# Kernel tuning notes

Measured on AMD Instinct MI355X. Metric: run time of the kernel, lower is better.

Reference implementation:

```python
import jax, jax.numpy as jnp
import numpy as np

B, C, N = 32, 128, 64
HID = 2 * C
STEEPNESS = 50.0


def _bitonic_layers(n):
    """Index pairs (a, b) for each compare-exchange layer of a bitonic sorting
    network, matching diffsort's bitonic_network construction."""
    num_blocks = int(np.log2(n))
    assert n == 2 ** num_blocks
    layers = []
    for block in range(num_blocks):
        for layer in range(block + 1):
            m = 2 ** (block - layer)
            a_idx, b_idx = [], []
            for i in range(0, n, 2 * m):
                for j in range(m):
                    ix = i + j
                    a, b = ix, ix + m
                    # alternate direction within bitonic blocks
                    if (ix // 2 ** (block + 1)) % 2 == 1:
                        a, b = b, a
                    a_idx.append(a)
                    b_idx.append(b)
            layers.append((np.asarray(a_idx), np.asarray(b_idx)))
    return layers

_LAYERS = _bitonic_layers(N)  # 21 layers for N=64


def _diff_sort(scores):
    """Differentiable bitonic sort (diffsort, distribution='cauchy').
    Returns (soft-sorted scores, soft permutation matrix P) with
    sorted = scores @ P; the module applies P via bmm(P, rows)."""
    b, n = scores.shape
    x = scores
    P = jnp.broadcast_to(jnp.eye(n, dtype=scores.dtype), (b, n, n))
    inv_pi = 1.0 / np.pi
    for a_idx, b_idx in _LAYERS:
        xa, xb = x[:, a_idx], x[:, b_idx]
        alpha = jnp.arctan((xb - xa) * STEEPNESS) * inv_pi + 0.5  # Cauchy CDF
        x = x.at[:, a_idx].set(alpha * xa + (1.0 - alpha) * xb)
        x = x.at[:, b_idx].set((1.0 - alpha) * xa + alpha * xb)
        Pa, Pb = P[:, :, a_idx], P[:, :, b_idx]
        al = alpha[:, None, :]
        P = P.at[:, :, a_idx].set(al * Pa + (1.0 - al) * Pb)
        P = P.at[:, :, b_idx].set((1.0 - al) * Pa + al * Pb)
    return x, P


def setup_inputs() -> dict:
    key = jax.random.key(0)
    ks = jax.random.split(key, 9)
    s = 0.05  # keep score magnitudes reasonable under steepness=50
    return {
        "x": jax.random.normal(ks[0], (B, C, N, N), jnp.float32),
        "w1": jax.random.normal(ks[1], (HID, C), jnp.float32) * s,
        "b1": jax.random.normal(ks[2], (HID,), jnp.float32) * s,
        "w2": jax.random.normal(ks[3], (HID, HID), jnp.float32) * s,
        "b2": jax.random.normal(ks[4], (HID,), jnp.float32) * s,
        "w_row": jax.random.normal(ks[5], (HID, N), jnp.float32) * s,
        "b_row": jax.random.normal(ks[6], (1,), jnp.float32) * s,
        "w_col": jax.random.normal(ks[7], (HID, N), jnp.float32) * s,
        "b_col": jax.random.normal(ks[8], (1,), jnp.float32) * s,
    }


def reference(x, w1, b1, w2, b2, w_row, b_row, w_col, b_col):
    # feat_extractor: two 1x1 convs (pointwise channel GEMMs) + ReLU
    h = jax.nn.relu(jnp.einsum('bchw,oc->bohw', x, w1) + b1[None, :, None, None])
    h = jax.nn.relu(jnp.einsum('bchw,oc->bohw', h, w2) + b2[None, :, None, None])

    # row branch: Conv1d(HID*N,1,1) over flattened (channel, width) per row
    row_scores = jnp.einsum('bchw,cw->bh', h, w_row) + b_row  # (B, N)
    _, p_row = _diff_sort(row_scores)
    x = jnp.einsum('bij,bcjk->bcik', p_row, x)  # bmm(P_row, x) per channel

    # col branch: Conv1d(HID*N,1,1) over flattened (channel, height) per column
    col_scores = jnp.einsum('bchw,ch->bw', h, w_col) + b_col  # (B, N)
    _, p_col = _diff_sort(col_scores)
    # original: bmm(P_col, x^T) then view as (B,C,N,N) with NO transpose back
    x = jnp.einsum('bij,bckj->bcik', p_col, x)
    return x
```

## Files before the change

### kernel.cpp

```cpp
#include <hip/hip_runtime.h>
#include <math.h>

#define B_    32
#define C_    128
#define N_    64
#define HID_  256
#define PIX_  4096
#define STEEP 50.0f
#define INV_PI 0.318309886183790671f
#define LDH   272
#define LDX   72

typedef unsigned short u16;
typedef __attribute__((ext_vector_type(8))) short bf16x8;
typedef __attribute__((ext_vector_type(4))) float f32x4;

__device__ __forceinline__ u16 f2bf(float f) {
    unsigned int u = __builtin_bit_cast(unsigned int, f);
    unsigned int r = (u + 0x7FFFu + ((u >> 16) & 1u)) >> 16;
    return (u16)r;
}
__device__ __forceinline__ float bf2f(u16 h) {
    unsigned int u = ((unsigned int)h) << 16;
    return __builtin_bit_cast(float, u);
}
__device__ __forceinline__ int h1_idx(int p, int k) {
    return p * LDH + (((k >> 3) + (p & 7)) & 31) * 8 + (k & 7);
}
__device__ __forceinline__ int x_idx(int p, int k) {
    return p * LDH + 128 + (((k >> 3) + (p & 7)) & 15) * 8 + (k & 7);
}

__global__ void k_prep(const float* __restrict__ w1, const float* __restrict__ w2,
                       u16* __restrict__ w1h, u16* __restrict__ w1l,
                       u16* __restrict__ w2h, u16* __restrict__ w2l,
                       float* __restrict__ col_s, const float* __restrict__ b_col) {
    int i = blockIdx.x * 256 + threadIdx.x;
    if (i < B_ * N_) col_s[i] = b_col[0];
    if (i < HID_ * C_) {
        float v = w1[i];
        u16 h = f2bf(v);
        w1h[i] = h;
        w1l[i] = f2bf(v - bf2f(h));
    } else {
        int j = i - HID_ * C_;
        if (j < HID_ * HID_) {
            float v = w2[j];
            u16 h = f2bf(v);
            w2h[j] = h;
            w2l[j] = f2bf(v - bf2f(h));
        }
    }
}

__global__ __launch_bounds__(256) void k12_fused(
    const float* __restrict__ x,
    const u16* __restrict__ w1h, const u16* __restrict__ w1l,
    const float* __restrict__ b1,
    const u16* __restrict__ w2h, const u16* __restrict__ w2l,
    const float* __restrict__ b2, const float* __restrict__ w_row,
    const float* __restrict__ b_row, const float* __restrict__ w_col,
    float* __restrict__ row_s, float* __restrict__ col_s) {
    __shared__ __align__(16) u16 Lh[64 * LDH];
    __shared__ __align__(16) u16 Ll[64 * LDH];
    __shared__ float col_red[64];
    __shared__ float row_red;

    const int t = threadIdx.x;
    const int l = t & 63, w = t >> 6;
    const int col = l & 15, q = l >> 4;
    const int hrow = blockIdx.x;
    const int b = blockIdx.y;
    const float* xb = x + (size_t)b * C_ * PIX_ + hrow * 64;

    if (t < 64) col_red[t] = 0.f;
    if (t == 0) row_red = 0.f;

    {
        const int pt = t & 15, ct = t >> 4;
#pragma unroll
        for (int cc = 0; cc < 4; cc++) {
            const int c = cc * 32 + 2 * ct;
            float4 v0 = *(const float4*)&xb[(size_t)c * PIX_ + pt * 4];
            float4 v1 = *(const float4*)&xb[(size_t)(c + 1) * PIX_ + pt * 4];
            float a0[4] = {v0.x, v0.y, v0.z, v0.w};
            float a1[4] = {v1.x, v1.y, v1.z, v1.w};
#pragma unroll
            for (int j = 0; j < 4; j++) {
                int p = pt * 4 + j;
                u16 h0 = f2bf(a0[j]), h1v = f2bf(a1[j]);
                u16 l0 = f2bf(a0[j] - bf2f(h0)), l1 = f2bf(a1[j] - bf2f(h1v));
                int idx = x_idx(p, c);
                *(unsigned int*)&Lh[idx] = (unsigned int)h0 | ((unsigned int)h1v << 16);
                *(unsigned int*)&Ll[idx] = (unsigned int)l0 | ((unsigned int)l1 << 16);
            }
        }
    }
    __syncthreads();

    f32x4 acc[4][4];
#pragma unroll
    for (int i = 0; i < 4; i++)
#pragma unroll
        for (int j = 0; j < 4; j++) acc[i][j] = (f32x4){0.f, 0.f, 0.f, 0.f};

    bf16x8 ah[4], al_[4];
#pragma unroll
    for (int mf = 0; mf < 4; mf++) {
        size_t ro = (size_t)(64 * w + 16 * mf + col) * C_ + q * 8;
        ah[mf] = *(const bf16x8*)&w1h[ro];
        al_[mf] = *(const bf16x8*)&w1l[ro];
    }
#pragma unroll
    for (int kc = 0; kc < 4; kc++) {
        bf16x8 bh[4], bl[4];
#pragma unroll
        for (int nt = 0; nt < 4; nt++) {
            int idx = x_idx(nt * 16 + col, kc * 32 + q * 8);
            bh[nt] = *(const bf16x8*)&Lh[idx];
            bl[nt] = *(const bf16x8*)&Ll[idx];
        }
        bf16x8 ahn[4], aln[4];
        const int kn = (kc + 1) & 3;
#pragma unroll
        for (int mf = 0; mf < 4; mf++) {
            size_t ro = (size_t)(64 * w + 16 * mf + col) * C_ + kn * 32 + q * 8;
            ahn[mf] = *(const bf16x8*)&w1h[ro];
            aln[mf] = *(const bf16x8*)&w1l[ro];
        }
#pragma unroll
        for (int mf = 0; mf < 4; mf++)
#pragma unroll
            for (int nt = 0; nt < 4; nt++) {
                acc[mf][nt] = __builtin_amdgcn_mfma_f32_16x16x32_bf16(ah[mf], bh[nt], acc[mf][nt], 0, 0, 0);
                acc[mf][nt] = __builtin_amdgcn_mfma_f32_16x16x32_bf16(ah[mf], bl[nt], acc[mf][nt], 0, 0, 0);
                acc[mf][nt] = __builtin_amdgcn_mfma_f32_16x16x32_bf16(al_[mf], bh[nt], acc[mf][nt], 0, 0, 0);
            }
#pragma unroll
        for (int mf = 0; mf < 4; mf++) { ah[mf] = ahn[mf]; al_[mf] = aln[mf]; }
    }

    bf16x8 ah2[4], al2[4];
#pragma unroll
    for (int mf = 0; mf < 4; mf++) {
        size_t ro = (size_t)(64 * w + 16 * mf + col) * HID_ + q * 8;
        ah2[mf] = *(const bf16x8*)&w2h[ro];
        al2[mf] = *(const bf16x8*)&w2l[ro];
    }
    __syncthreads();

#pragma unroll
    for (int mf = 0; mf < 4; mf++) {
        int o = 64 * w + 16 * mf + q * 4;
        float bias[4];
#pragma unroll
        for (int r = 0; r < 4; r++) bias[r] = b1[o + r];
#pragma unroll
        for (int nt = 0; nt < 4; nt++) {
            int p = nt * 16 + col;
            u16 hh[4], ll[4];
#pragma unroll
            for (int r = 0; r < 4; r++) {
                float v = fmaxf(acc[mf][nt][r] + bias[r], 0.f);
                u16 h = f2bf(v);
                hh[r] = h;
                ll[r] = f2bf(v - bf2f(h));
            }
            int idx = h1_idx(p, o);
            *(unsigned long long*)&Lh[idx] =
                (unsigned long long)hh[0] | ((unsigned long long)hh[1] << 16) |
                ((unsigned long long)hh[2] << 32) | ((unsigned long long)hh[3] << 48);
            *(unsigned long long*)&Ll[idx] =
                (unsigned long long)ll[0] | ((unsigned long long)ll[1] << 16) |
                ((unsigned long long)ll[2] << 32) | ((unsigned long long)ll[3] << 48);
        }
    }
    __syncthreads();

    f32x4 acc2[4][4];
#pragma unroll
    for (int i = 0; i < 4; i++)
#pragma unroll
        for (int j = 0; j < 4; j++) acc2[i][j] = (f32x4){0.f, 0.f, 0.f, 0.f};

#pragma unroll
    for (int kc = 0; kc < 8; kc++) {
        bf16x8 bh[4], bl[4];
#pragma unroll
        for (int nt = 0; nt < 4; nt++) {
            int idx = h1_idx(nt * 16 + col, kc * 32 + q * 8);
            bh[nt] = *(const bf16x8*)&Lh[idx];
            bl[nt] = *(const bf16x8*)&Ll[idx];
        }
        bf16x8 ahn[4], aln[4];
        const int kn = (kc + 1) & 7;
#pragma unroll
        for (int mf = 0; mf < 4; mf++) {
            size_t ro = (size_t)(64 * w + 16 * mf + col) * HID_ + kn * 32 + q * 8;
            ahn[mf] = *(const bf16x8*)&w2h[ro];
            aln[mf] = *(const bf16x8*)&w2l[ro];
        }
#pragma unroll
        for (int mf = 0; mf < 4; mf++)
#pragma unroll
            for (int nt = 0; nt < 4; nt++) {
                acc2[mf][nt] = __builtin_amdgcn_mfma_f32_16x16x32_bf16(ah2[mf], bh[nt], acc2[mf][nt], 0, 0, 0);
                acc2[mf][nt] = __builtin_amdgcn_mfma_f32_16x16x32_bf16(ah2[mf], bl[nt], acc2[mf][nt], 0, 0, 0);
                acc2[mf][nt] = __builtin_amdgcn_mfma_f32_16x16x32_bf16(al2[mf], bh[nt], acc2[mf][nt], 0, 0, 0);
            }
#pragma unroll
        for (int mf = 0; mf < 4; mf++) { ah2[mf] = ahn[mf]; al2[mf] = aln[mf]; }
    }

    float rpart = 0.f;
    float cpart[4] = {0.f, 0.f, 0.f, 0.f};
#pragma unroll
    for (int mf = 0; mf < 4; mf++) {
        int o = 64 * w + 16 * mf + q * 4;
#pragma unroll
        for (int r = 0; r < 4; r++) {
            float bias = b2[o + r];
            float wcv = w_col[(o + r) * N_ + hrow];
#pragma unroll
            for (int nt = 0; nt < 4; nt++) {
                int wc = nt * 16 + col;
                float v = fmaxf(acc2[mf][nt][r] + bias, 0.f);
                rpart += v * w_row[(o + r) * N_ + wc];
                cpart[nt] += v * wcv;
            }
        }
    }
#pragma unroll
    for (int off = 32; off; off >>= 1) rpart += __shfl_xor(rpart, off, 64);
    if (l == 0) atomicAdd(&row_red, rpart);
#pragma unroll
    for (int nt = 0; nt < 4; nt++) {
        float cp = cpart[nt];
        cp += __shfl_xor(cp, 16, 64);
        cp += __shfl_xor(cp, 32, 64);
        if (l < 16) atomicAdd(&col_red[nt * 16 + l], cp);
    }
    __syncthreads();
    if (t < 64) atomicAdd(&col_s[b * N_ + t], col_red[t]);
    if (t == 0) row_s[b * N_ + hrow] = b_row[0] + row_red;
}

__global__ __launch_bounds__(256) void k4_diffsort(const float* __restrict__ row_s,
                                                   const float* __restrict__ col_s,
                                                   u16* __restrict__ prow_h, u16* __restrict__ prow_l,
                                                   u16* __restrict__ pcol_h, u16* __restrict__ pcol_l) {
    const int t = threadIdx.x;
    const int lane = t & 63, w = t >> 6;
    const int which = blockIdx.x & 1;
    const int b = blockIdx.x >> 1;
    const float* sc = which ? col_s : row_s;
    u16* Ph = which ? pcol_h : prow_h;
    u16* Pl = which ? pcol_l : prow_l;

    float xv = sc[b * 64 + lane];
    float P[16];
#pragma unroll
    for (int r = 0; r < 16; r++) P[r] = ((w * 16 + r) == lane) ? 1.f : 0.f;

#pragma unroll
    for (int bl = 0; bl < 6; bl++) {
#pragma unroll
        for (int ly = 0; ly <= bl; ly++) {
            const int sh = bl - ly;
            const int m = 1 << sh;
            float xp = __shfl_xor(xv, m, 64);
            int lower = ((lane >> sh) & 1) ^ 1;
            int swp = (lane >> (bl + 1)) & 1;
            float diff = (lower ^ swp) ? (xp - xv) : (xv - xp);
            float al = atanf(diff * STEEP) * INV_PI + 0.5f;
            xv = al * xv + (1.f - al) * xp;
#pragma unroll
            for (int r = 0; r < 16; r++) {
                float Pp = __shfl_xor(P[r], m, 64);
                P[r] = al * P[r] + (1.f - al) * Pp;
            }
        }
    }
#pragma unroll
    for (int r = 0; r < 16; r++) {
        float v = P[r];
        u16 h = f2bf(v);
        int row = w * 16 + r;
        Ph[(size_t)b * 4096 + row * 64 + lane] = h;
        Pl[(size_t)b * 4096 + row * 64 + lane] = f2bf(v - bf2f(h));
    }
}

__global__ __launch_bounds__(256) void k5_permute(const float* __restrict__ x,
                                                  const u16* __restrict__ pcol_h,
                                                  const u16* __restrict__ pcol_l,
                                                  const u16* __restrict__ prow_h,
                                                  const u16* __restrict__ prow_l,
                                                  float* __restrict__ out) {
    __shared__ __align__(16) u16 Xh[64 * LDX];
    __shared__ __align__(16) u16 Xl[64 * LDX];
    __shared__ __align__(16) u16 Zh[64 * LDX];
    __shared__ __align__(16) u16 Zl[64 * LDX];
    const int t = threadIdx.x;
    const int l = t & 63, w = t >> 6;
    const int col = l & 15, q = l >> 4;
    const int b = blockIdx.y;
    const int cbase = blockIdx.x * 4;
    const int i0 = w * 16;

    const u16* pch = pcol_h + (size_t)b * 4096;
    const u16* pcl = pcol_l + (size_t)b * 4096;
    const u16* prh = prow_h + (size_t)b * 4096;
    const u16* prl = prow_l + (size_t)b * 4096;

    bf16x8 pcA_h[2], pcA_l[2];
#pragma unroll
    for (int ks = 0; ks < 2; ks++) {
        pcA_h[ks] = *(const bf16x8*)&pch[(i0 + col) * 64 + q * 8 + ks * 32];
        pcA_l[ks] = *(const bf16x8*)&pcl[(i0 + col) * 64 + q * 8 + ks * 32];
    }

    float4 pv[4];
    {
        const float* xc0 = x + ((size_t)b * C_ + cbase) * PIX_;
#pragma unroll
        for (int k = 0; k < 4; k++) pv[k] = *(const float4*)&xc0[(t + k * 256) * 4];
    }

    for (int ci = 0; ci < 4; ci++) {
#pragma unroll
        for (int k = 0; k < 4; k++) {
            int f = t + k * 256;
            int rw = f >> 4, c4 = f & 15;
            float4 v = pv[k];
            u16 h0 = f2bf(v.x), h1 = f2bf(v.y), h2 = f2bf(v.z), h3 = f2bf(v.w);
            ushort4 hv = {h0, h1, h2, h3};
            ushort4 lv = {f2bf(v.x - bf2f(h0)), f2bf(v.y - bf2f(h1)),
                          f2bf(v.z - bf2f(h2)), f2bf(v.w - bf2f(h3))};
            *(ushort4*)&Xh[rw * LDX + c4 * 4] = hv;
            *(ushort4*)&Xl[rw * LDX + c4 * 4] = lv;
        }
        __syncthreads();

        if (ci < 3) {
            const float* xcn = x + ((size_t)b * C_ + cbase + ci + 1) * PIX_;
#pragma unroll
            for (int k = 0; k < 4; k++) pv[k] = *(const float4*)&xcn[(t + k * 256) * 4];
        }

        f32x4 acc[4];
#pragma unroll
        for (int nt = 0; nt < 4; nt++) acc[nt] = (f32x4){0.f, 0.f, 0.f, 0.f};
#pragma unroll
        for (int ks = 0; ks < 2; ks++) {
            bf16x8 ah = pcA_h[ks], al_ = pcA_l[ks];
#pragma unroll
            for (int nt = 0; nt < 4; nt++) {
                bf16x8 bh = *(const bf16x8*)&Xh[(nt * 16 + col) * LDX + q * 8 + ks * 32];
                bf16x8 bl = *(const bf16x8*)&Xl[(nt * 16 + col) * LDX + q * 8 + ks * 32];
                acc[nt] = __builtin_amdgcn_mfma_f32_16x16x32_bf16(ah, bh, acc[nt], 0, 0, 0);
                acc[nt] = __builtin_amdgcn_mfma_f32_16x16x32_bf16(ah, bl, acc[nt], 0, 0, 0);
                acc[nt] = __builtin_amdgcn_mfma_f32_16x16x32_bf16(al_, bh, acc[nt], 0, 0, 0);
            }
        }
#pragma unroll
        for (int nt = 0; nt < 4; nt++)
#pragma unroll
            for (int r = 0; r < 4; r++) {
                float v = acc[nt][r];
                u16 h = f2bf(v);
                int rw = i0 + q * 4 + r;
                Zh[rw * LDX + nt * 16 + col] = h;
                Zl[rw * LDX + nt * 16 + col] = f2bf(v - bf2f(h));
            }

        f32x4 acc2[4];
#pragma unroll
        for (int nt = 0; nt < 4; nt++) acc2[nt] = (f32x4){0.f, 0.f, 0.f, 0.f};
#pragma unroll
        for (int ks = 0; ks < 2; ks++) {
            bf16x8 ah = *(const bf16x8*)&Zh[(i0 + col) * LDX + q * 8 + ks * 32];
            bf16x8 al_ = *(const bf16x8*)&Zl[(i0 + col) * LDX + q * 8 + ks * 32];
#pragma unroll
            for (int nt = 0; nt < 4; nt++) {
                bf16x8 bh = *(const bf16x8*)&prh[(nt * 16 + col) * 64 + q * 8 + ks * 32];
                bf16x8 bl = *(const bf16x8*)&prl[(nt * 16 + col) * 64 + q * 8 + ks * 32];
                acc2[nt] = __builtin_amdgcn_mfma_f32_16x16x32_bf16(ah, bh, acc2[nt], 0, 0, 0);
                acc2[nt] = __builtin_amdgcn_mfma_f32_16x16x32_bf16(ah, bl, acc2[nt], 0, 0, 0);
                acc2[nt] = __builtin_amdgcn_mfma_f32_16x16x32_bf16(al_, bh, acc2[nt], 0, 0, 0);
            }
        }
        float* oc = out + ((size_t)b * C_ + cbase + ci) * PIX_;
#pragma unroll
        for (int nt = 0; nt < 4; nt++)
#pragma unroll
            for (int r = 0; r < 4; r++)
                oc[(i0 + q * 4 + r) * 64 + nt * 16 + col] = acc2[nt][r];
        __syncthreads();
    }
}

extern "C" void kernel_launch(void* const* d_in, const int* in_sizes, int n_in,
                              void* d_out, int out_size, void* d_ws, size_t ws_size,
                              hipStream_t stream) {
    const float* x = (const float*)d_in[0];
    const float* w1 = (const float*)d_in[1];
    const float* b1 = (const float*)d_in[2];
    const float* w2 = (const float*)d_in[3];
    const float* b2 = (const float*)d_in[4];
    const float* w_row = (const float*)d_in[5];
    const float* b_row = (const float*)d_in[6];
    const float* w_col = (const float*)d_in[7];
    const float* b_col = (const float*)d_in[8];
    float* out = (float*)d_out;

    char* ws = (char*)d_ws;
    u16* w1h = (u16*)(ws);
    u16* w1l = (u16*)(ws + 65536);
    u16* w2h = (u16*)(ws + 131072);
    u16* w2l = (u16*)(ws + 262144);
    float* row_s = (float*)(ws + 393216);
    float* col_s = (float*)(ws + 401408);
    u16* prow_h = (u16*)(ws + 409600);
    u16* prow_l = (u16*)(ws + 671744);
    u16* pcol_h = (u16*)(ws + 933888);
    u16* pcol_l = (u16*)(ws + 1196032);

    hipLaunchKernelGGL(k_prep, dim3(384), dim3(256), 0, stream, w1, w2, w1h, w1l, w2h, w2l,
                       col_s, b_col);
    hipLaunchKernelGGL(k12_fused, dim3(64, 32), dim3(256), 0, stream,
                       x, w1h, w1l, b1, w2h, w2l, b2, w_row, b_row, w_col, row_s, col_s);
    hipLaunchKernelGGL(k4_diffsort, dim3(64), dim3(256), 0, stream,
                       row_s, col_s, prow_h, prow_l, pcol_h, pcol_l);
    hipLaunchKernelGGL(k5_permute, dim3(32, 32), dim3(256), 0, stream,
                       x, pcol_h, pcol_l, prow_h, prow_l, out);
}
```

Measured before the change: 275.9 us.

## Use 512-thread blocks in fused MLP and transpose MFMA operands in permute

The fused feature/score kernel now runs 8 waves per block, each owning 32 output channels instead of 64, which halves per-thread accumulators and spreads the MFMA work across more waves. The permute kernel swaps MFMA operand order so results land as contiguous rows, allowing packed 64-bit LDS writes and float4 global stores. It also hoists the row-permutation fragments into registers and drops the software prefetch of the next channel's x. The risks are higher register pressure in the permute kernel, loss of load/compute overlap from removing the prefetch, and extra LDS contention from more waves per block.

```diff
diff --git a/kernel.cpp b/kernel.cpp
--- a/kernel.cpp
+++ b/kernel.cpp
@@ -53,7 +53,7 @@
     }
 }
 
-__global__ __launch_bounds__(256) void k12_fused(
+__global__ __launch_bounds__(512) void k12_fused(
     const float* __restrict__ x,
     const u16* __restrict__ w1h, const u16* __restrict__ w1l,
     const float* __restrict__ b1,
@@ -79,8 +79,8 @@
     {
         const int pt = t & 15, ct = t >> 4;
 #pragma unroll
-        for (int cc = 0; cc < 4; cc++) {
-            const int c = cc * 32 + 2 * ct;
+        for (int cc = 0; cc < 2; cc++) {
+            const int c = cc * 64 + 2 * ct;
             float4 v0 = *(const float4*)&xb[(size_t)c * PIX_ + pt * 4];
             float4 v1 = *(const float4*)&xb[(size_t)(c + 1) * PIX_ + pt * 4];
             float a0[4] = {v0.x, v0.y, v0.z, v0.w};
@@ -98,16 +98,16 @@
     }
     __syncthreads();
 
-    f32x4 acc[4][4];
-#pragma unroll
-    for (int i = 0; i < 4; i++)
+    f32x4 acc[2][4];
+#pragma unroll
+    for (int i = 0; i < 2; i++)
 #pragma unroll
         for (int j = 0; j < 4; j++) acc[i][j] = (f32x4){0.f, 0.f, 0.f, 0.f};
 
-    bf16x8 ah[4], al_[4];
-#pragma unroll
-    for (int mf = 0; mf < 4; mf++) {
-        size_t ro = (size_t)(64 * w + 16 * mf + col) * C_ + q * 8;
+    bf16x8 ah[2], al_[2];
+#pragma unroll
+    for (int mf = 0; mf < 2; mf++) {
+        size_t ro = (size_t)(32 * w + 16 * mf + col) * C_ + q * 8;
         ah[mf] = *(const bf16x8*)&w1h[ro];
         al_[mf] = *(const bf16x8*)&w1l[ro];
     }
@@ -120,16 +120,16 @@
             bh[nt] = *(const bf16x8*)&Lh[idx];
             bl[nt] = *(const bf16x8*)&Ll[idx];
         }
-        bf16x8 ahn[4], aln[4];
+        bf16x8 ahn[2], aln[2];
         const int kn = (kc + 1) & 3;
 #pragma unroll
-        for (int mf = 0; mf < 4; mf++) {
-            size_t ro = (size_t)(64 * w + 16 * mf + col) * C_ + kn * 32 + q * 8;
+        for (int mf = 0; mf < 2; mf++) {
+            size_t ro = (size_t)(32 * w + 16 * mf + col) * C_ + kn * 32 + q * 8;
             ahn[mf] = *(const bf16x8*)&w1h[ro];
             aln[mf] = *(const bf16x8*)&w1l[ro];
         }
 #pragma unroll
-        for (int mf = 0; mf < 4; mf++)
+        for (int mf = 0; mf < 2; mf++)
 #pragma unroll
             for (int nt = 0; nt < 4; nt++) {
                 acc[mf][nt] = __builtin_amdgcn_mfma_f32_16x16x32_bf16(ah[mf], bh[nt], acc[mf][nt], 0, 0, 0);
@@ -137,21 +137,21 @@
                 acc[mf][nt] = __builtin_amdgcn_mfma_f32_16x16x32_bf16(al_[mf], bh[nt], acc[mf][nt], 0, 0, 0);
             }
 #pragma unroll
-        for (int mf = 0; mf < 4; mf++) { ah[mf] = ahn[mf]; al_[mf] = aln[mf]; }
-    }
-
-    bf16x8 ah2[4], al2[4];
-#pragma unroll
-    for (int mf = 0; mf < 4; mf++) {
-        size_t ro = (size_t)(64 * w + 16 * mf + col) * HID_ + q * 8;
+        for (int mf = 0; mf < 2; mf++) { ah[mf] = ahn[mf]; al_[mf] = aln[mf]; }
+    }
+
+    bf16x8 ah2[2], al2[2];
+#pragma unroll
+    for (int mf = 0; mf < 2; mf++) {
+        size_t ro = (size_t)(32 * w + 16 * mf + col) * HID_ + q * 8;
         ah2[mf] = *(const bf16x8*)&w2h[ro];
         al2[mf] = *(const bf16x8*)&w2l[ro];
     }
     __syncthreads();
 
 #pragma unroll
-    for (int mf = 0; mf < 4; mf++) {
-        int o = 64 * w + 16 * mf + q * 4;
+    for (int mf = 0; mf < 2; mf++) {
+        int o = 32 * w + 16 * mf + q * 4;
         float bias[4];
 #pragma unroll
         for (int r = 0; r < 4; r++) bias[r] = b1[o + r];
@@ -177,9 +177,9 @@
     }
     __syncthreads();
 
-    f32x4 acc2[4][4];
-#pragma unroll
-    for (int i = 0; i < 4; i++)
+    f32x4 acc2[2][4];
+#pragma unroll
+    for (int i = 0; i < 2; i++)
 #pragma unroll
         for (int j = 0; j < 4; j++) acc2[i][j] = (f32x4){0.f, 0.f, 0.f, 0.f};
 
@@ -192,16 +192,16 @@
             bh[nt] = *(const bf16x8*)&Lh[idx];
             bl[nt] = *(const bf16x8*)&Ll[idx];
         }
-        bf16x8 ahn[4], aln[4];
+        bf16x8 ahn[2], aln[2];
         const int kn = (kc + 1) & 7;
 #pragma unroll
-        for (int mf = 0; mf < 4; mf++) {
-            size_t ro = (size_t)(64 * w + 16 * mf + col) * HID_ + kn * 32 + q * 8;
+        for (int mf = 0; mf < 2; mf++) {
+            size_t ro = (size_t)(32 * w + 16 * mf + col) * HID_ + kn * 32 + q * 8;
             ahn[mf] = *(const bf16x8*)&w2h[ro];
             aln[mf] = *(const bf16x8*)&w2l[ro];
         }
 #pragma unroll
-        for (int mf = 0; mf < 4; mf++)
+        for (int mf = 0; mf < 2; mf++)
 #pragma unroll
             for (int nt = 0; nt < 4; nt++) {
                 acc2[mf][nt] = __builtin_amdgcn_mfma_f32_16x16x32_bf16(ah2[mf], bh[nt], acc2[mf][nt], 0, 0, 0);
@@ -209,14 +209,14 @@
                 acc2[mf][nt] = __builtin_amdgcn_mfma_f32_16x16x32_bf16(al2[mf], bh[nt], acc2[mf][nt], 0, 0, 0);
             }
 #pragma unroll
-        for (int mf = 0; mf < 4; mf++) { ah2[mf] = ahn[mf]; al2[mf] = aln[mf]; }
+        for (int mf = 0; mf < 2; mf++) { ah2[mf] = ahn[mf]; al2[mf] = aln[mf]; }
     }
 
     float rpart = 0.f;
     float cpart[4] = {0.f, 0.f, 0.f, 0.f};
 #pragma unroll
-    for (int mf = 0; mf < 4; mf++) {
-        int o = 64 * w + 16 * mf + q * 4;
+    for (int mf = 0; mf < 2; mf++) {
+        int o = 32 * w + 16 * mf + q * 4;
 #pragma unroll
         for (int r = 0; r < 4; r++) {
             float bias = b2[o + r];
@@ -319,20 +319,23 @@
         pcA_h[ks] = *(const bf16x8*)&pch[(i0 + col) * 64 + q * 8 + ks * 32];
         pcA_l[ks] = *(const bf16x8*)&pcl[(i0 + col) * 64 + q * 8 + ks * 32];
     }
-
-    float4 pv[4];
-    {
-        const float* xc0 = x + ((size_t)b * C_ + cbase) * PIX_;
-#pragma unroll
-        for (int k = 0; k < 4; k++) pv[k] = *(const float4*)&xc0[(t + k * 256) * 4];
-    }
+    bf16x8 prA_h[2][4], prA_l[2][4];
+#pragma unroll
+    for (int ks = 0; ks < 2; ks++)
+#pragma unroll
+        for (int ntj = 0; ntj < 4; ntj++) {
+            prA_h[ks][ntj] = *(const bf16x8*)&prh[(ntj * 16 + col) * 64 + q * 8 + ks * 32];
+            prA_l[ks][ntj] = *(const bf16x8*)&prl[(ntj * 16 + col) * 64 + q * 8 + ks * 32];
+        }
 
     for (int ci = 0; ci < 4; ci++) {
+        const int c = cbase + ci;
+        const float* xc = x + ((size_t)b * C_ + c) * PIX_;
 #pragma unroll
         for (int k = 0; k < 4; k++) {
             int f = t + k * 256;
             int rw = f >> 4, c4 = f & 15;
-            float4 v = pv[k];
+            float4 v = *(const float4*)&xc[f * 4];
             u16 h0 = f2bf(v.x), h1 = f2bf(v.y), h2 = f2bf(v.z), h3 = f2bf(v.w);
             ushort4 hv = {h0, h1, h2, h3};
             ushort4 lv = {f2bf(v.x - bf2f(h0)), f2bf(v.y - bf2f(h1)),
@@ -342,60 +345,60 @@
         }
         __syncthreads();
 
-        if (ci < 3) {
-            const float* xcn = x + ((size_t)b * C_ + cbase + ci + 1) * PIX_;
-#pragma unroll
-            for (int k = 0; k < 4; k++) pv[k] = *(const float4*)&xcn[(t + k * 256) * 4];
-        }
-
         f32x4 acc[4];
 #pragma unroll
         for (int nt = 0; nt < 4; nt++) acc[nt] = (f32x4){0.f, 0.f, 0.f, 0.f};
 #pragma unroll
         for (int ks = 0; ks < 2; ks++) {
-            bf16x8 ah = pcA_h[ks], al_ = pcA_l[ks];
+            bf16x8 ph = pcA_h[ks], pl = pcA_l[ks];
 #pragma unroll
             for (int nt = 0; nt < 4; nt++) {
-                bf16x8 bh = *(const bf16x8*)&Xh[(nt * 16 + col) * LDX + q * 8 + ks * 32];
-                bf16x8 bl = *(const bf16x8*)&Xl[(nt * 16 + col) * LDX + q * 8 + ks * 32];
-                acc[nt] = __builtin_amdgcn_mfma_f32_16x16x32_bf16(ah, bh, acc[nt], 0, 0, 0);
-                acc[nt] = __builtin_amdgcn_mfma_f32_16x16x32_bf16(ah, bl, acc[nt], 0, 0, 0);
-                acc[nt] = __builtin_amdgcn_mfma_f32_16x16x32_bf16(al_, bh, acc[nt], 0, 0, 0);
-            }
-        }
-#pragma unroll
-        for (int nt = 0; nt < 4; nt++)
+                bf16x8 xh8 = *(const bf16x8*)&Xh[(nt * 16 + col) * LDX + q * 8 + ks * 32];
+                bf16x8 xl8 = *(const bf16x8*)&Xl[(nt * 16 + col) * LDX + q * 8 + ks * 32];
+                acc[nt] = __builtin_amdgcn_mfma_f32_16x16x32_bf16(xh8, ph, acc[nt], 0, 0, 0);
+                acc[nt] = __builtin_amdgcn_mfma_f32_16x16x32_bf16(xl8, ph, acc[nt], 0, 0, 0);
+                acc[nt] = __builtin_amdgcn_mfma_f32_16x16x32_bf16(xh8, pl, acc[nt], 0, 0, 0);
+            }
+        }
+#pragma unroll
+        for (int nt = 0; nt < 4; nt++) {
+            u16 hh[4], ll[4];
 #pragma unroll
             for (int r = 0; r < 4; r++) {
                 float v = acc[nt][r];
                 u16 h = f2bf(v);
-                int rw = i0 + q * 4 + r;
-                Zh[rw * LDX + nt * 16 + col] = h;
-                Zl[rw * LDX + nt * 16 + col] = f2bf(v - bf2f(h));
-            }
+                hh[r] = h;
+                ll[r] = f2bf(v - bf2f(h));
+            }
+            int zi = (i0 + col) * LDX + nt * 16 + q * 4;
+            *(unsigned long long*)&Zh[zi] =
+                (unsigned long long)hh[0] | ((unsigned long long)hh[1] << 16) |
+                ((unsigned long long)hh[2] << 32) | ((unsigned long long)hh[3] << 48);
+            *(unsigned long long*)&Zl[zi] =
+                (unsigned long long)ll[0] | ((unsigned long long)ll[1] << 16) |
+                ((unsigned long long)ll[2] << 32) | ((unsigned long long)ll[3] << 48);
+        }
 
         f32x4 acc2[4];
 #pragma unroll
         for (int nt = 0; nt < 4; nt++) acc2[nt] = (f32x4){0.f, 0.f, 0.f, 0.f};
 #pragma unroll
         for (int ks = 0; ks < 2; ks++) {
-            bf16x8 ah = *(const bf16x8*)&Zh[(i0 + col) * LDX + q * 8 + ks * 32];
-            bf16x8 al_ = *(const bf16x8*)&Zl[(i0 + col) * LDX + q * 8 + ks * 32];
-#pragma unroll
-            for (int nt = 0; nt < 4; nt++) {
-                bf16x8 bh = *(const bf16x8*)&prh[(nt * 16 + col) * 64 + q * 8 + ks * 32];
-                bf16x8 bl = *(const bf16x8*)&prl[(nt * 16 + col) * 64 + q * 8 + ks * 32];
-                acc2[nt] = __builtin_amdgcn_mfma_f32_16x16x32_bf16(ah, bh, acc2[nt], 0, 0, 0);
-                acc2[nt] = __builtin_amdgcn_mfma_f32_16x16x32_bf16(ah, bl, acc2[nt], 0, 0, 0);
-                acc2[nt] = __builtin_amdgcn_mfma_f32_16x16x32_bf16(al_, bh, acc2[nt], 0, 0, 0);
-            }
-        }
-        float* oc = out + ((size_t)b * C_ + cbase + ci) * PIX_;
-#pragma unroll
-        for (int nt = 0; nt < 4; nt++)
-#pragma unroll
-            for (int r = 0; r < 4; r++)
-                oc[(i0 + q * 4 + r) * 64 + nt * 16 + col] = acc2[nt][r];
+            bf16x8 zh8 = *(const bf16x8*)&Zh[(i0 + col) * LDX + q * 8 + ks * 32];
+            bf16x8 zl8 = *(const bf16x8*)&Zl[(i0 + col) * LDX + q * 8 + ks * 32];
+#pragma unroll
+            for (int ntj = 0; ntj < 4; ntj++) {
+                acc2[ntj] = __builtin_amdgcn_mfma_f32_16x16x32_bf16(prA_h[ks][ntj], zh8, acc2[ntj], 0, 0, 0);
+                acc2[ntj] = __builtin_amdgcn_mfma_f32_16x16x32_bf16(prA_l[ks][ntj], zh8, acc2[ntj], 0, 0, 0);
+                acc2[ntj] = __builtin_amdgcn_mfma_f32_16x16x32_bf16(prA_h[ks][ntj], zl8, acc2[ntj], 0, 0, 0);
+            }
+        }
+        float* oc = out + ((size_t)b * C_ + c) * PIX_;
+#pragma unroll
+        for (int ntj = 0; ntj < 4; ntj++) {
+            float4 vv = {acc2[ntj][0], acc2[ntj][1], acc2[ntj][2], acc2[ntj][3]};
+            *(float4*)&oc[(i0 + col) * 64 + ntj * 16 + q * 4] = vv;
+        }
         __syncthreads();
     }
 }
@@ -428,7 +431,7 @@
 
     hipLaunchKernelGGL(k_prep, dim3(384), dim3(256), 0, stream, w1, w2, w1h, w1l, w2h, w2l,
                        col_s, b_col);
-    hipLaunchKernelGGL(k12_fused, dim3(64, 32), dim3(256), 0, stream,
+    hipLaunchKernelGGL(k12_fused, dim3(64, 32), dim3(512), 0, stream,
                        x, w1h, w1l, b1, w2h, w2l, b2, w_row, b_row, w_col, row_s, col_s);
     hipLaunchKernelGGL(k4_diffsort, dim3(64), dim3(256), 0, stream,
                        row_s, col_s, prow_h, prow_l, pcol_h, pcol_l);
```

Result: faster. 269.7 us (-2.2%).
